# Optimization experiments

Measured on AMD Instinct MI355X. Metric: run time of the kernel, lower is better.

## Reference

```python
import jax, jax.numpy as jnp
import numpy as np

ALPHA = 0.2  # leaky relu slope
NEG = -1e9


def setup_inputs() -> dict:
    key = jax.random.key(0)
    ks = jax.random.split(key, 8)
    B, N, F_IN, H, HID, OUT = 2, 4096, 512, 4, 128, 64
    x = jax.random.normal(ks[0], (B, N, F_IN), dtype=jnp.float32)
    adj = jax.random.randint(ks[1], (B, N, N), 0, 2, dtype=jnp.int32)
    s_in = float(np.sqrt(2.0 / (F_IN + HID)))
    W_heads = jax.random.normal(ks[2], (H, HID, F_IN), dtype=jnp.float32) * s_in
    a1_heads = jax.random.normal(ks[3], (H, HID), dtype=jnp.float32) * 0.1
    a2_heads = jax.random.normal(ks[4], (H, HID), dtype=jnp.float32) * 0.1
    s_out = float(np.sqrt(2.0 / (H * HID + OUT)))
    W_out = jax.random.normal(ks[5], (OUT, H * HID), dtype=jnp.float32) * s_out
    a1_out = jax.random.normal(ks[6], (OUT,), dtype=jnp.float32) * 0.1
    a2_out = jax.random.normal(ks[7], (OUT,), dtype=jnp.float32) * 0.1
    return {"x": x, "adj": adj, "W_heads": W_heads, "a1_heads": a1_heads,
            "a2_heads": a2_heads, "W_out": W_out, "a1_out": a1_out, "a2_out": a2_out}


def _gat_layer(x, adj, W, a1, a2, concat):
    # x: [B,N,F], W: [O,F], a1/a2: [O]
    h = jnp.einsum('bnf,of->bno', x, W)            # [B,N,O]
    f1 = jnp.einsum('bno,o->bn', h, a1)            # [B,N]
    f2 = jnp.einsum('bno,o->bn', h, a2)            # [B,N]
    e = f1[:, :, None] + f2[:, None, :]            # [B,N,N] additive scores
    e = jnp.where(e > 0, e, ALPHA * e)             # leaky relu
    e = jnp.where(adj == 0, NEG, e)                # adjacency mask
    att = jax.nn.softmax(e, axis=2)
    h_prime = jnp.einsum('bnm,bmo->bno', att, h)
    return jax.nn.elu(h_prime) if concat else h_prime


def reference(x, adj, W_heads, a1_heads, a2_heads, W_out, a1_out, a2_out):
    H = W_heads.shape[0]
    heads = [_gat_layer(x, adj, W_heads[i], a1_heads[i], a2_heads[i], True)
             for i in range(H)]
    x_cat = jnp.concatenate(heads, axis=2)         # [B,N,H*HID]
    return _gat_layer(x_cat, adj, W_out, a1_out, a2_out, False)
```

## Files before the change

kernel.cpp:

```cpp
#include <hip/hip_runtime.h>

#define TB 2
#define TN 4096
#define TH 4
#define THID 128
#define TOUT 64
#define NW 128

using f4    = __attribute__((ext_vector_type(4))) float;
using s16x8 = __attribute__((ext_vector_type(8))) short;
using s16x4 = __attribute__((ext_vector_type(4))) short;
using u32x4 = __attribute__((ext_vector_type(4))) unsigned;

static __device__ __forceinline__ short f2bf(float f){
  unsigned u = __float_as_uint(f);
  unsigned r = u + 0x7FFFu + ((u >> 16) & 1u);
  return (short)(r >> 16);
}
static __device__ __forceinline__ float bf2f(short s){
  return __uint_as_float(((unsigned)(unsigned short)s) << 16);
}
static __device__ __forceinline__ unsigned encf(float f){
  unsigned u = __float_as_uint(f);
  return (u & 0x80000000u) ? ~u : (u | 0x80000000u);
}
static __device__ __forceinline__ float decf(unsigned u){
  unsigned v = (u & 0x80000000u) ? (u & 0x7FFFFFFFu) : ~u;
  return __uint_as_float(v);
}
static __device__ __forceinline__ void gll16(const void* g, void* l){
  __builtin_amdgcn_global_load_lds((const __attribute__((address_space(1))) unsigned int*)g,
                                   (__attribute__((address_space(3))) unsigned int*)l, 16, 0, 0);
}
static __device__ __forceinline__ f4 mfma_bf16(s16x8 a, s16x8 b, f4 c){
  return __builtin_amdgcn_mfma_f32_16x16x32_bf16(a, b, c, 0, 0, 0);
}

__global__ __launch_bounds__(256) void k_pack(const int* __restrict__ adj,
                                              unsigned* __restrict__ adjp){
  int lane = threadIdx.x & 63, w = threadIdx.x >> 6;
  int gw0 = (blockIdx.x*4 + w)*64;
  const int4* base = (const int4*)adj + (size_t)gw0*8;
  int4 v[8];
#pragma unroll
  for (int i = 0; i < 8; ++i) v[i] = base[i*64 + lane];
  unsigned nib[8];
#pragma unroll
  for (int i = 0; i < 8; ++i){
    unsigned nb = (v[i].x != 0 ? 1u : 0u) | (v[i].y != 0 ? 2u : 0u)
                | (v[i].z != 0 ? 4u : 0u) | (v[i].w != 0 ? 8u : 0u);
    nib[i] = nb << (4*(lane & 7));
  }
#pragma unroll
  for (int i = 0; i < 8; ++i){
    nib[i] |= __shfl_xor(nib[i], 1);
    nib[i] |= __shfl_xor(nib[i], 2);
    nib[i] |= __shfl_xor(nib[i], 4);
  }
  if ((lane & 7) == 0){
    int sub = lane >> 3;
#pragma unroll
    for (int i = 0; i < 8; ++i)
      adjp[gw0 + i*8 + sub] = nib[i];
  }
}

__global__ void k_prep(unsigned* __restrict__ mx,
                       const float* __restrict__ x, short* __restrict__ xh, short* __restrict__ xl,
                       const float* __restrict__ Wh, short* __restrict__ wh, short* __restrict__ wl,
                       const float* __restrict__ Wo, short* __restrict__ wo){
  int bid = blockIdx.x, tid = threadIdx.x;
  if (bid == 0 && tid < 16) mx[tid] = 0;
  if (bid < 4096){
    int t = bid * 256 + tid;
    f4 v = ((const f4*)x)[t];
    s16x4 h, l;
#pragma unroll
    for (int e = 0; e < 4; ++e){
      short hb = f2bf(v[e]);
      h[e] = hb;
      l[e] = f2bf(v[e] - bf2f(hb));
    }
    ((s16x4*)xh)[t] = h;
    ((s16x4*)xl)[t] = l;
  } else if (bid < 4352){
    int t = (bid - 4096) * 256 + tid;
    f4 v = ((const f4*)Wh)[t];
    s16x4 h, l;
#pragma unroll
    for (int e = 0; e < 4; ++e){
      short hb = f2bf(v[e]);
      h[e] = hb;
      l[e] = f2bf(v[e] - bf2f(hb));
    }
    ((s16x4*)wh)[t] = h;
    ((s16x4*)wl)[t] = l;
  } else {
    int t = (bid - 4352) * 256 + tid;
    f4 v = ((const f4*)Wo)[t];
    s16x4 h;
#pragma unroll
    for (int e = 0; e < 4; ++e) h[e] = f2bf(v[e]);
    ((s16x4*)wo)[t] = h;
  }
}

__global__ __launch_bounds__(512, 2) void k_gemm1(
    const short* __restrict__ xh, const short* __restrict__ xl,
    const short* __restrict__ wh, const short* __restrict__ wl,
    const float* __restrict__ a1h, const float* __restrict__ a2h,
    short* __restrict__ hTb, float* __restrict__ f1g,
    float* __restrict__ Qa, float* __restrict__ Sa, unsigned* __restrict__ mx){
  __shared__ short tiles[2][4][8192];
  __shared__ float red[2][128][2];
  __shared__ float bmx[2];
  int tid = threadIdx.x, lane = tid & 63, w = tid >> 6;
  int kgrp = lane >> 4, li = lane & 15;
  int nblk = blockIdx.x >> 6, mblk = blockIdx.x & 63;
  int n0 = nblk * 128, m0 = mblk * 128;
  int wn = w >> 2, wm = w & 3;
  const f4 fz = {0.f, 0.f, 0.f, 0.f};
  f4 acc[4][2];
#pragma unroll
  for (int i = 0; i < 4; ++i)
#pragma unroll
    for (int j = 0; j < 2; ++j) acc[i][j] = fz;

#pragma unroll
  for (int tno = 0; tno < 4; ++tno){
    const short* gb = (tno==0 ? wh : tno==1 ? wl : tno==2 ? xh : xl);
    int r0 = (tno < 2) ? n0 : m0;
#pragma unroll
    for (int i = 0; i < 2; ++i){
      int s = (i*8 + w)*64 + lane;
      int row = s >> 3, c = s & 7, cs = c ^ (row & 7);
      gll16(gb + (size_t)(r0 + row)*512 + cs*8, (char*)tiles[0][tno] + (i*8+w)*1024);
    }
  }
  asm volatile("s_waitcnt vmcnt(0)" ::: "memory");
  __syncthreads();

  for (int kt = 0; kt < 8; ++kt){
    int cur = kt & 1;
    if (kt < 7){
      int k0 = (kt+1) * 64;
#pragma unroll
      for (int tno = 0; tno < 4; ++tno){
        const short* gb = (tno==0 ? wh : tno==1 ? wl : tno==2 ? xh : xl);
        int r0 = (tno < 2) ? n0 : m0;
#pragma unroll
        for (int i = 0; i < 2; ++i){
          int s = (i*8 + w)*64 + lane;
          int row = s >> 3, c = s & 7, cs = c ^ (row & 7);
          gll16(gb + (size_t)(r0 + row)*512 + k0 + cs*8, (char*)tiles[cur^1][tno] + (i*8+w)*1024);
        }
      }
    }
    const char* t0 = (const char*)tiles[cur][0];
    const char* t1 = (const char*)tiles[cur][1];
    const char* t2 = (const char*)tiles[cur][2];
    const char* t3 = (const char*)tiles[cur][3];
#pragma unroll
    for (int ks = 0; ks < 2; ++ks){
      int ck = ks*4 + kgrp;
      s16x8 ah[4], al[4], bh[2], bl[2];
#pragma unroll
      for (int fn = 0; fn < 4; ++fn){
        int row = wn*64 + fn*16 + li;
        int off = row*128 + ((ck ^ (row & 7)) << 4);
        ah[fn] = *(const s16x8*)(t0 + off);
        al[fn] = *(const s16x8*)(t1 + off);
      }
#pragma unroll
      for (int fm = 0; fm < 2; ++fm){
        int row = wm*32 + fm*16 + li;
        int off = row*128 + ((ck ^ (row & 7)) << 4);
        bh[fm] = *(const s16x8*)(t2 + off);
        bl[fm] = *(const s16x8*)(t3 + off);
      }
#pragma unroll
      for (int fn = 0; fn < 4; ++fn)
#pragma unroll
        for (int fm = 0; fm < 2; ++fm)
          acc[fn][fm] = mfma_bf16(ah[fn], bh[fm], acc[fn][fm]);
#pragma unroll
      for (int fn = 0; fn < 4; ++fn)
#pragma unroll
        for (int fm = 0; fm < 2; ++fm)
          acc[fn][fm] = mfma_bf16(ah[fn], bl[fm], acc[fn][fm]);
#pragma unroll
      for (int fn = 0; fn < 4; ++fn)
#pragma unroll
        for (int fm = 0; fm < 2; ++fm)
          acc[fn][fm] = mfma_bf16(al[fn], bh[fm], acc[fn][fm]);
    }
    asm volatile("s_waitcnt vmcnt(0)" ::: "memory");
    __syncthreads();
  }
  int head = nblk;
#pragma unroll
  for (int fn = 0; fn < 4; ++fn){
#pragma unroll
    for (int fm = 0; fm < 2; ++fm){
#pragma unroll
      for (int r = 0; r < 4; ++r){
        int nout = n0 + wn*64 + fn*16 + kgrp*4 + r;
        int m = m0 + wm*32 + fm*16 + li;
        int b = m >> 12, n = m & 4095;
        int hid = nout & 127;
        size_t idx = ((size_t)((b*TH + head)*THID + hid))*TN + n;
        hTb[idx] = f2bf(acc[fn][fm][r]);
      }
    }
  }
  const float* a1p = a1h + head*THID;
  const float* a2p = a2h + head*THID;
  float s1[2] = {0.f, 0.f}, s2[2] = {0.f, 0.f};
#pragma unroll
  for (int fn = 0; fn < 4; ++fn)
#pragma unroll
    for (int r = 0; r < 4; ++r){
      int row = wn*64 + fn*16 + kgrp*4 + r;
      float w1 = a1p[row], w2 = a2p[row];
#pragma unroll
      for (int fm = 0; fm < 2; ++fm){
        s1[fm] = fmaf(acc[fn][fm][r], w1, s1[fm]);
        s2[fm] = fmaf(acc[fn][fm][r], w2, s2[fm]);
      }
    }
#pragma unroll
  for (int fm = 0; fm < 2; ++fm){
    s1[fm] += __shfl_xor(s1[fm], 16); s1[fm] += __shfl_xor(s1[fm], 32);
    s2[fm] += __shfl_xor(s2[fm], 16); s2[fm] += __shfl_xor(s2[fm], 32);
  }
  if (kgrp == 0){
#pragma unroll
    for (int fm = 0; fm < 2; ++fm){
      int col = wm*32 + fm*16 + li;
      red[wn][col][0] = s1[fm];
      red[wn][col][1] = s2[fm];
    }
  }
  __syncthreads();
  if (tid < 128){
    float f1v = red[0][tid][0] + red[1][tid][0];
    float f2v = red[0][tid][1] + red[1][tid][1];
    int m = m0 + tid, b = m >> 12, n = m & 4095;
    int idx = (b*TH + head)*TN + n;
    f1g[idx] = f1v;
    Qa[idx] = expf(f2v);
    Sa[idx] = expf(0.2f*f2v);
    float wmx = f2v;
#pragma unroll
    for (int d = 1; d < 64; d <<= 1) wmx = fmaxf(wmx, __shfl_xor(wmx, d));
    if ((tid & 63) == 0) bmx[tid >> 6] = wmx;
  }
  __syncthreads();
  if (tid == 0){
    int b = m0 >> 12;
    atomicMax(&mx[b*TH + head], encf(fmaxf(bmx[0], bmx[1])));
  }
}

__global__ __launch_bounds__(256, 2) void k_attn1(
    const short* __restrict__ hTb, const float* __restrict__ f1,
    const float* __restrict__ Qa, const float* __restrict__ Sa,
    const unsigned* __restrict__ adjp, const unsigned* __restrict__ mx,
    short* __restrict__ part, float* __restrict__ sums){
  __shared__ short tile[2][8192];
  __shared__ float Qs[1024], Ss[1024];
  int tid = threadIdx.x, lane = tid & 63, w = tid >> 6;
  int kgrp = lane >> 4, li = lane & 15;
  int bid = blockIdx.x;
  int js = bid >> 7, b = (bid >> 6) & 1, h = (bid >> 4) & 3, rblk = bid & 15;
  int bh = b*TH + h;
  int jbase = js * 1024;
  int r0b = rblk * 256;
  const short* hbase = hTb + ((size_t)bh*THID)*TN;
  const float* Qrow = Qa + (size_t)bh*TN + jbase;
  const float* Srow = Sa + (size_t)bh*TN + jbase;

  auto STAGE = [&](int t, char* dst){
    int jg = jbase + t*64;
#pragma unroll
    for (int i = 0; i < 4; ++i){
      int s = (i*4 + w)*64 + lane;
      int row = s >> 3, c = s & 7, cs = c ^ (row & 7);
      gll16(hbase + (size_t)row*TN + jg + cs*8, dst + (i*4+w)*1024);
    }
  };

  gll16(Qrow + w*256 + lane*4, (char*)Qs + w*1024);
  gll16(Srow + w*256 + lane*4, (char*)Ss + w*1024);
  STAGE(0, (char*)tile[0]);

  int r0 = r0b + w*64;
  float Pv[4], Rv[4];
  int rowa[4];
  float mf = decf(mx[bh]);
#pragma unroll
  for (int rf = 0; rf < 4; ++rf){
    int row = r0 + rf*16 + li;
    rowa[rf] = row;
    float f1v = f1[bh*TN + row];
    float e = f1v + mf;
    float m = e > 0.f ? e : 0.2f*e;
    Pv[rf] = expf(f1v - m);
    Rv[rf] = expf(0.2f*f1v - m);
  }
  const f4 fz = {0.f,0.f,0.f,0.f};
  f4 acc[4][8];
#pragma unroll
  for (int i = 0; i < 4; ++i)
#pragma unroll
    for (int j = 0; j < 8; ++j) acc[i][j] = fz;
  f4 accs[4] = {fz, fz, fz, fz};
  s16x8 ones;
#pragma unroll
  for (int e = 0; e < 8; ++e) ones[e] = (short)0x3F80;

  uint2 awc[4], awn[4];
#pragma unroll
  for (int rf = 0; rf < 4; ++rf)
    awc[rf] = *(const uint2*)&adjp[(size_t)(b*TN + rowa[rf])*NW + (jbase >> 5)];

  asm volatile("s_waitcnt vmcnt(0)" ::: "memory");
  __syncthreads();

  for (int jt = 0; jt < 16; ++jt){
    int cur = jt & 1;
    if (jt < 15){
      STAGE(jt+1, (char*)tile[cur^1]);
      int jg = jbase + (jt+1)*64;
#pragma unroll
      for (int rf = 0; rf < 4; ++rf)
        awn[rf] = *(const uint2*)&adjp[(size_t)(b*TN + rowa[rf])*NW + (jg >> 5)];
    }
    int j0 = jt*64;
    const char* tp = (const char*)tile[cur];
#pragma unroll
    for (int ks = 0; ks < 2; ++ks){
      int jloc = j0 + ks*32 + kgrp*8;
      float qv[8], sv[8];
      *(f4*)&qv[0] = *(const f4*)&Qs[jloc];
      *(f4*)&qv[4] = *(const f4*)&Qs[jloc+4];
      *(f4*)&sv[0] = *(const f4*)&Ss[jloc];
      *(f4*)&sv[4] = *(const f4*)&Ss[jloc+4];
      s16x8 af[4];
#pragma unroll
      for (int rf = 0; rf < 4; ++rf){
        unsigned word = ks ? awc[rf].y : awc[rf].x;
        unsigned byt = (word >> (kgrp*8)) & 0xFFu;
        float P = Pv[rf], R = Rv[rf];
        u32x4 pw;
#pragma unroll
        for (int pe = 0; pe < 4; ++pe){
          float va = fmaxf(P*qv[2*pe],   R*sv[2*pe]);
          float vb = fmaxf(P*qv[2*pe+1], R*sv[2*pe+1]);
          va = (byt & (1u << (2*pe)))   ? va : 0.f;
          vb = (byt & (1u << (2*pe+1))) ? vb : 0.f;
          unsigned ua = __float_as_uint(va) + 0x8000u;
          unsigned ub = __float_as_uint(vb) + 0x8000u;
          pw[pe] = __builtin_amdgcn_perm(ub, ua, 0x07060302);
        }
        af[rf] = __builtin_bit_cast(s16x8, pw);
      }
#pragma unroll
      for (int rf = 0; rf < 4; ++rf)
        accs[rf] = mfma_bf16(af[rf], ones, accs[rf]);
#pragma unroll
      for (int cf = 0; cf < 8; ++cf){
        int col = cf*16 + li;
        int off = col*128 + (((ks*4 + kgrp) ^ (col & 7)) << 4);
        s16x8 bfr = *(const s16x8*)(tp + off);
#pragma unroll
        for (int rf = 0; rf < 4; ++rf)
          acc[rf][cf] = mfma_bf16(af[rf], bfr, acc[rf][cf]);
      }
    }
    asm volatile("s_waitcnt vmcnt(0)" ::: "memory");
    __syncthreads();
#pragma unroll
    for (int rf = 0; rf < 4; ++rf) awc[rf] = awn[rf];
  }
  int sl = js*8 + bh;
  if (li == 0){
#pragma unroll
    for (int rf = 0; rf < 4; ++rf)
#pragma unroll
      for (int r = 0; r < 4; ++r)
        sums[(size_t)sl*TN + r0 + rf*16 + kgrp*4 + r] = accs[rf][r];
  }
#pragma unroll
  for (int rf = 0; rf < 4; ++rf)
#pragma unroll
    for (int cf = 0; cf < 8; ++cf)
#pragma unroll
      for (int r = 0; r < 4; ++r){
        int row = r0 + rf*16 + kgrp*4 + r;
        int hid = cf*16 + li;
        part[((size_t)sl*TN + row)*THID + hid] = f2bf(acc[rf][cf][r]);
      }
}

__global__ __launch_bounds__(128) void k_cg2(
    const short* __restrict__ part1, const float* __restrict__ sums1,
    const short* __restrict__ wo,
    const float* __restrict__ a1o, const float* __restrict__ a2o,
    short* __restrict__ h2T, float* __restrict__ f1o,
    float* __restrict__ Q2, float* __restrict__ S2, unsigned* __restrict__ mx2){
  __shared__ short xs[32*512];
  int tid = threadIdx.x, lane = tid & 63, w = tid >> 6;
  int kgrp = lane >> 4, li = lane & 15;
  int m0 = blockIdx.x * 32;
  for (int it = 0; it < 16; ++it){
    int idx = it*128 + tid;
    int r = idx >> 6, c8 = idx & 63;
    int row = m0 + r, b = row >> 12, n = row & 4095;
    int h = c8 >> 4, hid8 = c8 & 15;
    float a[8] = {0,0,0,0,0,0,0,0};
    float s = 0.f;
#pragma unroll
    for (int js = 0; js < 4; ++js){
      size_t rowoff = (size_t)(js*8 + b*TH + h)*TN + n;
      s16x8 pv = *(const s16x8*)(part1 + rowoff*THID + hid8*8);
#pragma unroll
      for (int e = 0; e < 8; ++e) a[e] += bf2f(pv[e]);
      s += sums1[rowoff];
    }
    float inv = 1.f / s;
    s16x8 o;
#pragma unroll
    for (int e = 0; e < 8; ++e){
      float xv = a[e] * inv;
      o[e] = f2bf(xv > 0.f ? xv : expm1f(xv));
    }
    *(s16x8*)((char*)xs + r*1024 + ((c8*16) ^ ((r & 7) << 4))) = o;
  }
  __syncthreads();
  const f4 fz = {0.f,0.f,0.f,0.f};
  f4 acc[4] = {fz, fz, fz, fz};
  int rowL = w*16 + li;
  for (int kt = 0; kt < 16; ++kt){
    int k = kt*32 + kgrp*8;
    s16x8 a = *(const s16x8*)((const char*)xs + rowL*1024 + ((k*2) ^ ((rowL & 7) << 4)));
#pragma unroll
    for (int cf = 0; cf < 4; ++cf){
      int col = cf*16 + li;
      s16x8 bfr = *(const s16x8*)(wo + (size_t)col*512 + k);
      acc[cf] = mfma_bf16(a, bfr, acc[cf]);
    }
  }
  float p1[4] = {0,0,0,0}, p2[4] = {0,0,0,0};
#pragma unroll
  for (int cf = 0; cf < 4; ++cf){
    int o = cf*16 + li;
    float w1 = a1o[o], w2 = a2o[o];
#pragma unroll
    for (int r = 0; r < 4; ++r){
      p1[r] = fmaf(acc[cf][r], w1, p1[r]);
      p2[r] = fmaf(acc[cf][r], w2, p2[r]);
    }
  }
#pragma unroll
  for (int r = 0; r < 4; ++r){
#pragma unroll
    for (int d = 1; d < 16; d <<= 1){
      p1[r] += __shfl_xor(p1[r], d);
      p2[r] += __shfl_xor(p2[r], d);
    }
  }
#pragma unroll
  for (int cf = 0; cf < 4; ++cf)
#pragma unroll
    for (int r = 0; r < 4; ++r){
      int row = m0 + w*16 + kgrp*4 + r;
      int o = cf*16 + li;
      int b = row >> 12, n = row & 4095;
      h2T[((size_t)(b*TOUT + o))*TN + n] = f2bf(acc[cf][r]);
    }
  if (li == 0){
#pragma unroll
    for (int r = 0; r < 4; ++r){
      int row = m0 + w*16 + kgrp*4 + r;
      f1o[row] = p1[r];
      Q2[row] = expf(p2[r]);
      S2[row] = expf(0.2f*p2[r]);
    }
  }
  float m2 = fmaxf(fmaxf(p2[0], p2[1]), fmaxf(p2[2], p2[3]));
  m2 = fmaxf(m2, __shfl_xor(m2, 16));
  m2 = fmaxf(m2, __shfl_xor(m2, 32));
  __shared__ float bm[2];
  if (lane == 0) bm[w] = m2;
  __syncthreads();
  if (tid == 0) atomicMax(&mx2[m0 >> 12], encf(fmaxf(bm[0], bm[1])));
}

__global__ __launch_bounds__(256, 2) void k_attn2(
    const short* __restrict__ h2T, const float* __restrict__ f1o,
    const float* __restrict__ Q2, const float* __restrict__ S2,
    const unsigned* __restrict__ adjp, const unsigned* __restrict__ mx2,
    float* __restrict__ part, float* __restrict__ sums){
  __shared__ short tile[2][4096];
  __shared__ float Qs[512], Ss[512];
  int tid = threadIdx.x, lane = tid & 63, w = tid >> 6;
  int kgrp = lane >> 4, li = lane & 15;
  int bid = blockIdx.x;
  int js = bid >> 6, b = (bid >> 5) & 1, rblk = bid & 31;
  int jbase = js * 512;
  int r0b = rblk * 128;
  const short* hbase = h2T + (size_t)b*TOUT*TN;
  const float* Qrow = Q2 + (size_t)b*TN + jbase;
  const float* Srow = S2 + (size_t)b*TN + jbase;

  auto STAGE = [&](int t, char* dst){
    int jg = jbase + t*64;
#pragma unroll
    for (int i = 0; i < 2; ++i){
      int s = (i*4 + w)*64 + lane;
      int row = s >> 3, c = s & 7, cs = c ^ (row & 7);
      gll16(hbase + (size_t)row*TN + jg + cs*8, dst + (i*4+w)*1024);
    }
  };

  if (w < 2) gll16(Qrow + w*256 + lane*4, (char*)Qs + w*1024);
  else       gll16(Srow + (w-2)*256 + lane*4, (char*)Ss + (w-2)*1024);
  STAGE(0, (char*)tile[0]);

  int r0 = r0b + w*32;
  float Pv[2], Rv[2];
  int rowa[2];
  float mf = decf(mx2[b]);
#pragma unroll
  for (int rf = 0; rf < 2; ++rf){
    int row = r0 + rf*16 + li;
    rowa[rf] = row;
    float f1v = f1o[b*TN + row];
    float e = f1v + mf;
    float m = e > 0.f ? e : 0.2f*e;
    Pv[rf] = expf(f1v - m);
    Rv[rf] = expf(0.2f*f1v - m);
  }
  const f4 fz = {0.f,0.f,0.f,0.f};
  f4 acc[2][4];
#pragma unroll
  for (int i = 0; i < 2; ++i)
#pragma unroll
    for (int j = 0; j < 4; ++j) acc[i][j] = fz;
  f4 accs[2] = {fz, fz};
  s16x8 ones;
#pragma unroll
  for (int e = 0; e < 8; ++e) ones[e] = (short)0x3F80;

  uint2 awc[2], awn[2];
#pragma unroll
  for (int rf = 0; rf < 2; ++rf)
    awc[rf] = *(const uint2*)&adjp[(size_t)(b*TN + rowa[rf])*NW + (jbase >> 5)];

  asm volatile("s_waitcnt vmcnt(0)" ::: "memory");
  __syncthreads();

  for (int jt = 0; jt < 8; ++jt){
    int cur = jt & 1;
    if (jt < 7){
      STAGE(jt+1, (char*)tile[cur^1]);
      int jg = jbase + (jt+1)*64;
#pragma unroll
      for (int rf = 0; rf < 2; ++rf)
        awn[rf] = *(const uint2*)&adjp[(size_t)(b*TN + rowa[rf])*NW + (jg >> 5)];
    }
    int j0 = jt*64;
    const char* tp = (const char*)tile[cur];
#pragma unroll
    for (int ks = 0; ks < 2; ++ks){
      int jloc = j0 + ks*32 + kgrp*8;
      float qv[8], sv[8];
      *(f4*)&qv[0] = *(const f4*)&Qs[jloc];
      *(f4*)&qv[4] = *(const f4*)&Qs[jloc+4];
      *(f4*)&sv[0] = *(const f4*)&Ss[jloc];
      *(f4*)&sv[4] = *(const f4*)&Ss[jloc+4];
      s16x8 af[2];
#pragma unroll
      for (int rf = 0; rf < 2; ++rf){
        unsigned word = ks ? awc[rf].y : awc[rf].x;
        unsigned byt = (word >> (kgrp*8)) & 0xFFu;
        float P = Pv[rf], R = Rv[rf];
        u32x4 pw;
#pragma unroll
        for (int pe = 0; pe < 4; ++pe){
          float va = fmaxf(P*qv[2*pe],   R*sv[2*pe]);
          float vb = fmaxf(P*qv[2*pe+1], R*sv[2*pe+1]);
          va = (byt & (1u << (2*pe)))   ? va : 0.f;
          vb = (byt & (1u << (2*pe+1))) ? vb : 0.f;
          unsigned ua = __float_as_uint(va) + 0x8000u;
          unsigned ub = __float_as_uint(vb) + 0x8000u;
          pw[pe] = __builtin_amdgcn_perm(ub, ua, 0x07060302);
        }
        af[rf] = __builtin_bit_cast(s16x8, pw);
      }
      accs[0] = mfma_bf16(af[0], ones, accs[0]);
      accs[1] = mfma_bf16(af[1], ones, accs[1]);
#pragma unroll
      for (int cf = 0; cf < 4; ++cf){
        int col = cf*16 + li;
        int off = col*128 + (((ks*4 + kgrp) ^ (col & 7)) << 4);
        s16x8 bfr = *(const s16x8*)(tp + off);
        acc[0][cf] = mfma_bf16(af[0], bfr, acc[0][cf]);
        acc[1][cf] = mfma_bf16(af[1], bfr, acc[1][cf]);
      }
    }
    asm volatile("s_waitcnt vmcnt(0)" ::: "memory");
    __syncthreads();
    awc[0] = awn[0]; awc[1] = awn[1];
  }
  int sl = js*2 + b;
  if (li == 0){
#pragma unroll
    for (int rf = 0; rf < 2; ++rf)
#pragma unroll
      for (int r = 0; r < 4; ++r)
        sums[(size_t)sl*TN + r0 + rf*16 + kgrp*4 + r] = accs[rf][r];
  }
#pragma unroll
  for (int rf = 0; rf < 2; ++rf)
#pragma unroll
    for (int cf = 0; cf < 4; ++cf)
#pragma unroll
      for (int r = 0; r < 4; ++r){
        int row = r0 + rf*16 + kgrp*4 + r;
        int o = cf*16 + li;
        part[((size_t)sl*TN + row)*TOUT + o] = acc[rf][cf][r];
      }
}

__global__ void k_comb2(const float* __restrict__ part, const float* __restrict__ sums,
                        float* __restrict__ out){
  int t = blockIdx.x*256 + threadIdx.x;
  int o4 = t & 15, n = (t >> 4) & 4095, b = t >> 16;
  f4 a = {0.f,0.f,0.f,0.f};
  float s = 0.f;
#pragma unroll
  for (int js = 0; js < 8; ++js){
    int sl = js*2 + b;
    a += ((const f4*)part)[((size_t)sl*TN + n)*16 + o4];
    s += sums[(size_t)sl*TN + n];
  }
  f4 r = a / s;
  ((f4*)out)[((size_t)(b*TN + n))*16 + o4] = r;
}

extern "C" void kernel_launch(void* const* d_in, const int* in_sizes, int n_in,
                              void* d_out, int out_size, void* d_ws, size_t ws_size,
                              hipStream_t stream) {
  (void)in_sizes; (void)n_in; (void)out_size; (void)ws_size;
  const float* x       = (const float*)d_in[0];
  const int*   adj     = (const int*)d_in[1];
  const float* W_heads = (const float*)d_in[2];
  const float* a1h     = (const float*)d_in[3];
  const float* a2h     = (const float*)d_in[4];
  const float* W_out   = (const float*)d_in[5];
  const float* a1o     = (const float*)d_in[6];
  const float* a2o     = (const float*)d_in[7];

  char* p = (char*)d_ws;
  auto alloc = [&](size_t sz){ char* r = p; p += (sz + 255) & ~(size_t)255; return r; };
  unsigned* adjp  = (unsigned*) alloc(4ull*1048576);
  short*    wo    = (short*)    alloc(2ull*32768);
  short*    hTb   = (short*)    alloc(2ull*4194304);
  float*    f1    = (float*)    alloc(4ull*32768);
  float*    Qa    = (float*)    alloc(4ull*32768);
  float*    Sa    = (float*)    alloc(4ull*32768);
  unsigned* mx    = (unsigned*) alloc(4ull*16);
  float*    f1o   = (float*)    alloc(4ull*8192);
  float*    Q2    = (float*)    alloc(4ull*8192);
  float*    S2    = (float*)    alloc(4ull*8192);
  short*    h2T   = (short*)    alloc(2ull*524288);
  float*    sums1 = (float*)    alloc(4ull*131072);
  float*    sums2 = (float*)    alloc(4ull*65536);
  char* A = alloc(33554432ull);
  short* xh   = (short*)A;
  short* xl   = (short*)(A + 8388608);
  short* part1 = (short*)A;
  char* Bu = alloc(16777216ull);
  short* wh = (short*)Bu;
  short* wl = (short*)(Bu + 524288);
  float* part2 = (float*)Bu;

  k_pack <<<4096, 256, 0, stream>>>(adj, adjp);
  k_prep <<<4384, 256, 0, stream>>>(mx, x, xh, xl, W_heads, wh, wl, W_out, wo);
  k_gemm1<<<256, 512, 0, stream>>>(xh, xl, wh, wl, a1h, a2h, hTb, f1, Qa, Sa, mx);
  k_attn1<<<512, 256, 0, stream>>>(hTb, f1, Qa, Sa, adjp, mx, part1, sums1);
  k_cg2  <<<256, 128, 0, stream>>>(part1, sums1, wo, a1o, a2o, h2T, f1o, Q2, S2, mx + 8);
  k_attn2<<<512, 256, 0, stream>>>(h2T, f1o, Q2, S2, adjp, mx + 8, part2, sums2);
  k_comb2<<<512, 256, 0, stream>>>(part2, sums2, (float*)d_out);
}
```

Measured before the change: 153.2 us.

## Fuse adjacency packing into prep kernel and single-buffer gemm1 LDS tiles

Folds the adjacency bit-packing kernel into the bf16 conversion prep kernel, so one launch does both and the inter-kernel gap goes away. In the first GEMM, the double-buffered LDS tiles become a single buffer that is loaded and then waited on every k-step. This halves shared memory use, which can allow more resident blocks per CU. The cost is that global loads no longer overlap the MFMA work.

```diff
diff --git a/kernel.cpp b/kernel.cpp
--- a/kernel.cpp
+++ b/kernel.cpp
@@ -36,43 +36,41 @@
   return __builtin_amdgcn_mfma_f32_16x16x32_bf16(a, b, c, 0, 0, 0);
 }
 
-__global__ __launch_bounds__(256) void k_pack(const int* __restrict__ adj,
-                                              unsigned* __restrict__ adjp){
-  int lane = threadIdx.x & 63, w = threadIdx.x >> 6;
-  int gw0 = (blockIdx.x*4 + w)*64;
-  const int4* base = (const int4*)adj + (size_t)gw0*8;
-  int4 v[8];
-#pragma unroll
-  for (int i = 0; i < 8; ++i) v[i] = base[i*64 + lane];
-  unsigned nib[8];
-#pragma unroll
-  for (int i = 0; i < 8; ++i){
-    unsigned nb = (v[i].x != 0 ? 1u : 0u) | (v[i].y != 0 ? 2u : 0u)
-                | (v[i].z != 0 ? 4u : 0u) | (v[i].w != 0 ? 8u : 0u);
-    nib[i] = nb << (4*(lane & 7));
-  }
-#pragma unroll
-  for (int i = 0; i < 8; ++i){
-    nib[i] |= __shfl_xor(nib[i], 1);
-    nib[i] |= __shfl_xor(nib[i], 2);
-    nib[i] |= __shfl_xor(nib[i], 4);
-  }
-  if ((lane & 7) == 0){
-    int sub = lane >> 3;
-#pragma unroll
-    for (int i = 0; i < 8; ++i)
-      adjp[gw0 + i*8 + sub] = nib[i];
-  }
-}
-
-__global__ void k_prep(unsigned* __restrict__ mx,
-                       const float* __restrict__ x, short* __restrict__ xh, short* __restrict__ xl,
-                       const float* __restrict__ Wh, short* __restrict__ wh, short* __restrict__ wl,
-                       const float* __restrict__ Wo, short* __restrict__ wo){
+__global__ __launch_bounds__(256) void k_prep(
+    const int* __restrict__ adj, unsigned* __restrict__ adjp, unsigned* __restrict__ mx,
+    const float* __restrict__ x, short* __restrict__ xh, short* __restrict__ xl,
+    const float* __restrict__ Wh, short* __restrict__ wh, short* __restrict__ wl,
+    const float* __restrict__ Wo, short* __restrict__ wo){
   int bid = blockIdx.x, tid = threadIdx.x;
   if (bid == 0 && tid < 16) mx[tid] = 0;
   if (bid < 4096){
-    int t = bid * 256 + tid;
+    int lane = tid & 63, w = tid >> 6;
+    int gw0 = (bid*4 + w)*64;
+    const int4* base = (const int4*)adj + (size_t)gw0*8;
+    int4 v[8];
+#pragma unroll
+    for (int i = 0; i < 8; ++i) v[i] = base[i*64 + lane];
+    unsigned nib[8];
+#pragma unroll
+    for (int i = 0; i < 8; ++i){
+      unsigned nb = (v[i].x != 0 ? 1u : 0u) | (v[i].y != 0 ? 2u : 0u)
+                  | (v[i].z != 0 ? 4u : 0u) | (v[i].w != 0 ? 8u : 0u);
+      nib[i] = nb << (4*(lane & 7));
+    }
+#pragma unroll
+    for (int i = 0; i < 8; ++i){
+      nib[i] |= __shfl_xor(nib[i], 1);
+      nib[i] |= __shfl_xor(nib[i], 2);
+      nib[i] |= __shfl_xor(nib[i], 4);
+    }
+    if ((lane & 7) == 0){
+      int sub = lane >> 3;
+#pragma unroll
+      for (int i = 0; i < 8; ++i)
+        adjp[gw0 + i*8 + sub] = nib[i];
+    }
+  } else if (bid < 8192){
+    int t = (bid - 4096) * 256 + tid;
     f4 v = ((const f4*)x)[t];
     s16x4 h, l;
 #pragma unroll
@@ -83,8 +81,8 @@
     }
     ((s16x4*)xh)[t] = h;
     ((s16x4*)xl)[t] = l;
-  } else if (bid < 4352){
-    int t = (bid - 4096) * 256 + tid;
+  } else if (bid < 8448){
+    int t = (bid - 8192) * 256 + tid;
     f4 v = ((const f4*)Wh)[t];
     s16x4 h, l;
 #pragma unroll
@@ -96,7 +94,7 @@
     ((s16x4*)wh)[t] = h;
     ((s16x4*)wl)[t] = l;
   } else {
-    int t = (bid - 4352) * 256 + tid;
+    int t = (bid - 8448) * 256 + tid;
     f4 v = ((const f4*)Wo)[t];
     s16x4 h;
 #pragma unroll
@@ -111,7 +109,7 @@
     const float* __restrict__ a1h, const float* __restrict__ a2h,
     short* __restrict__ hTb, float* __restrict__ f1g,
     float* __restrict__ Qa, float* __restrict__ Sa, unsigned* __restrict__ mx){
-  __shared__ short tiles[2][4][8192];
+  __shared__ short tiles[4][8192];
   __shared__ float red[2][128][2];
   __shared__ float bmx[2];
   int tid = threadIdx.x, lane = tid & 63, w = tid >> 6;
@@ -126,40 +124,26 @@
 #pragma unroll
     for (int j = 0; j < 2; ++j) acc[i][j] = fz;
 
-#pragma unroll
-  for (int tno = 0; tno < 4; ++tno){
-    const short* gb = (tno==0 ? wh : tno==1 ? wl : tno==2 ? xh : xl);
-    int r0 = (tno < 2) ? n0 : m0;
-#pragma unroll
-    for (int i = 0; i < 2; ++i){
-      int s = (i*8 + w)*64 + lane;
-      int row = s >> 3, c = s & 7, cs = c ^ (row & 7);
-      gll16(gb + (size_t)(r0 + row)*512 + cs*8, (char*)tiles[0][tno] + (i*8+w)*1024);
-    }
-  }
-  asm volatile("s_waitcnt vmcnt(0)" ::: "memory");
-  __syncthreads();
-
   for (int kt = 0; kt < 8; ++kt){
-    int cur = kt & 1;
-    if (kt < 7){
-      int k0 = (kt+1) * 64;
-#pragma unroll
-      for (int tno = 0; tno < 4; ++tno){
-        const short* gb = (tno==0 ? wh : tno==1 ? wl : tno==2 ? xh : xl);
-        int r0 = (tno < 2) ? n0 : m0;
-#pragma unroll
-        for (int i = 0; i < 2; ++i){
-          int s = (i*8 + w)*64 + lane;
-          int row = s >> 3, c = s & 7, cs = c ^ (row & 7);
-          gll16(gb + (size_t)(r0 + row)*512 + k0 + cs*8, (char*)tiles[cur^1][tno] + (i*8+w)*1024);
-        }
-      }
-    }
-    const char* t0 = (const char*)tiles[cur][0];
-    const char* t1 = (const char*)tiles[cur][1];
-    const char* t2 = (const char*)tiles[cur][2];
-    const char* t3 = (const char*)tiles[cur][3];
+    int k0 = kt * 64;
+    __syncthreads();
+#pragma unroll
+    for (int tno = 0; tno < 4; ++tno){
+      const short* gb = (tno==0 ? wh : tno==1 ? wl : tno==2 ? xh : xl);
+      int r0 = (tno < 2) ? n0 : m0;
+#pragma unroll
+      for (int i = 0; i < 2; ++i){
+        int s = (i*8 + w)*64 + lane;
+        int row = s >> 3, c = s & 7, cs = c ^ (row & 7);
+        gll16(gb + (size_t)(r0 + row)*512 + k0 + cs*8, (char*)tiles[tno] + (i*8+w)*1024);
+      }
+    }
+    asm volatile("s_waitcnt vmcnt(0)" ::: "memory");
+    __syncthreads();
+    const char* t0 = (const char*)tiles[0];
+    const char* t1 = (const char*)tiles[1];
+    const char* t2 = (const char*)tiles[2];
+    const char* t3 = (const char*)tiles[3];
 #pragma unroll
     for (int ks = 0; ks < 2; ++ks){
       int ck = ks*4 + kgrp;
@@ -194,8 +178,6 @@
         for (int fm = 0; fm < 2; ++fm)
           acc[fn][fm] = mfma_bf16(al[fn], bh[fm], acc[fn][fm]);
     }
-    asm volatile("s_waitcnt vmcnt(0)" ::: "memory");
-    __syncthreads();
   }
   int head = nblk;
 #pragma unroll
@@ -687,8 +669,7 @@
   short* wl = (short*)(Bu + 524288);
   float* part2 = (float*)Bu;
 
-  k_pack <<<4096, 256, 0, stream>>>(adj, adjp);
-  k_prep <<<4384, 256, 0, stream>>>(mx, x, xh, xl, W_heads, wh, wl, W_out, wo);
+  k_prep <<<8480, 256, 0, stream>>>(adj, adjp, mx, x, xh, xl, W_heads, wh, wl, W_out, wo);
   k_gemm1<<<256, 512, 0, stream>>>(xh, xl, wh, wl, a1h, a2h, hTb, f1, Qa, Sa, mx);
   k_attn1<<<512, 256, 0, stream>>>(hTb, f1, Qa, Sa, adjp, mx, part1, sums1);
   k_cg2  <<<256, 128, 0, stream>>>(part1, sums1, wo, a1o, a2o, h2T, f1o, Q2, S2, mx + 8);
```

Result: no change. 152.0 us (-0.7%).
